# Kernel optimization log

Measured on AMD Instinct MI355X. Metric: run time of the kernel, lower is better.

The kernel has to match this reference:

```python
import jax, jax.numpy as jnp
import numpy as np

N_NODES = 100000
N_EDGES = 3200000
D_FEAT = 128
HIDDEN = 32
N_CLASS = 2


def setup_inputs() -> dict:
    key = jax.random.key(0)
    k1, k2, k3, k4 = jax.random.split(key, 4)
    x = jax.random.normal(k1, (N_NODES, D_FEAT), dtype=jnp.float32)
    edge_index = jax.random.randint(k2, (2, N_EDGES), 0, N_NODES, dtype=jnp.int64)
    W1 = jax.random.normal(k3, (D_FEAT, HIDDEN), dtype=jnp.float32) * (1.0 / np.sqrt(D_FEAT))
    b1 = jnp.zeros((HIDDEN,), dtype=jnp.float32)
    W2 = jax.random.normal(k4, (HIDDEN, N_CLASS), dtype=jnp.float32) * (1.0 / np.sqrt(HIDDEN))
    b2 = jnp.zeros((N_CLASS,), dtype=jnp.float32)
    return {"x": x, "edge_index": edge_index, "W1": W1, "b1": b1, "W2": W2, "b2": b2}


def _gcn_conv(x, src, dst, norm, W, b, n_nodes):
    # Linear transform first (PyG GCNConv order), then gather-scale-scatter.
    h = x @ W                          # [N, out]
    msg = h[src] * norm[:, None]       # [E+N, out]
    out = jax.ops.segment_sum(msg, dst, num_segments=n_nodes)
    return out + b


def reference(x, edge_index, W1, b1, W2, b2):
    n_nodes = x.shape[0]
    # Add self-loops (GCNConv default add_self_loops=True)
    loop = jnp.arange(n_nodes, dtype=edge_index.dtype)
    src = jnp.concatenate([edge_index[0], loop])
    dst = jnp.concatenate([edge_index[1], loop])
    # Symmetric normalization D^{-1/2} (A+I) D^{-1/2}; degree counted on dst.
    deg = jax.ops.segment_sum(jnp.ones_like(dst, dtype=x.dtype), dst, num_segments=n_nodes)
    deg_inv_sqrt = jnp.where(deg > 0, jax.lax.rsqrt(deg), 0.0)
    norm = deg_inv_sqrt[src] * deg_inv_sqrt[dst]   # [E+N]
    h = jax.nn.relu(_gcn_conv(x, src, dst, norm, W1, b1, n_nodes))
    # F.dropout(training=False) in eval mode is identity.
    logits = _gcn_conv(h, src, dst, norm, W2, b2, n_nodes)
    return jax.nn.log_softmax(logits, axis=1)
```

## Files before the change

kernel.cpp:

```cpp
#include <hip/hip_runtime.h>
#include <hip/hip_fp16.h>

#define NN 100000
#define NE 3200000
#define DF 128
#define HID 32
#define NC 2
#define NBUK 782
#define CAP 5376
#define PEB 8192

typedef float floatx2 __attribute__((ext_vector_type(2)));

#if defined(__has_builtin)
#if __has_builtin(__builtin_amdgcn_cvt_pk_fp8_f32) && __has_builtin(__builtin_amdgcn_cvt_pk_f32_fp8)
#define HW_FP8 1
#endif
#endif
#ifndef HW_FP8
#define HW_FP8 0
#endif

#if !HW_FP8
__device__ inline float4 e4m3x4_f4(unsigned u) {
    unsigned w0 = ((u & 0x7fu) << 7) | ((u & 0x80u) << 8)
                | ((u & 0x7f00u) << 15) | ((u & 0x8000u) << 16);
    unsigned t = u >> 16;
    unsigned w1 = ((t & 0x7fu) << 7) | ((t & 0x80u) << 8)
                | ((t & 0x7f00u) << 15) | ((t & 0x8000u) << 16);
    __half2 h0 = *reinterpret_cast<__half2*>(&w0);
    __half2 h1 = *reinterpret_cast<__half2*>(&w1);
    __half2 k = __float2half2_rn(256.f);
    float2 f0 = __half22float2(__hmul2(h0, k));
    float2 f1 = __half22float2(__hmul2(h1, k));
    return make_float4(f0.x, f0.y, f1.x, f1.y);
}
__device__ inline unsigned f2e4m3(float f) {
    unsigned u = __float_as_uint(f);
    unsigned s = (u >> 24) & 0x80u;
    int e = (int)((u >> 23) & 0xffu);
    unsigned m = u & 0x7fffffu;
    int ee = e - 120;
    if (ee >= 16) return s | 0x7eu;
    if (ee <= 0) {
        int sh = 21 - ee;
        if (sh > 31) return s;
        unsigned q = ((0x800000u | m) + (1u << (sh - 1))) >> sh;
        return s | q;
    }
    unsigned q = (m + 0x80000u) >> 20;
    if (q == 8u) { q = 0u; if (++ee >= 16) return s | 0x7eu; }
    if (ee == 15 && q == 7u) return s | 0x7eu;
    return s | ((unsigned)ee << 3) | q;
}
#endif

__device__ inline unsigned pk4_fp8(float a, float b, float c, float d) {
#if HW_FP8
    int w = 0;
    w = __builtin_amdgcn_cvt_pk_fp8_f32(a, b, w, false);
    w = __builtin_amdgcn_cvt_pk_fp8_f32(c, d, w, true);
    return (unsigned)w;
#else
    return f2e4m3(a) | (f2e4m3(b) << 8) | (f2e4m3(c) << 16) | (f2e4m3(d) << 24);
#endif
}

__global__ void k_zc(int* __restrict__ cursor) {
    int i = threadIdx.x;
    if (i < NBUK) cursor[i] = i * CAP;
}

__global__ __launch_bounds__(1024) void k_part(const int* __restrict__ eidx,
                                               int* __restrict__ cursor,
                                               unsigned* __restrict__ scr) {
    __shared__ unsigned hist[NBUK];
    __shared__ unsigned lofs[NBUK + 1];
    __shared__ unsigned aux[NBUK];
    __shared__ unsigned stage[PEB];
    __shared__ int sm[1024];
    int tid = threadIdx.x;
    int base = blockIdx.x * PEB;

    if (tid < NBUK) hist[tid] = 0u;
    __syncthreads();

    int s[PEB / 1024], d[PEB / 1024];
#pragma unroll
    for (int i = 0; i < PEB / 1024; ++i) {
        int e = base + i * 1024 + tid;
        if (e < NE) {
            s[i] = eidx[e];
            d[i] = eidx[NE + e];
            atomicAdd(&hist[d[i] >> 7], 1u);
        } else d[i] = -1;
    }
    __syncthreads();

    int v = (tid < NBUK) ? (int)hist[tid] : 0;
    sm[tid] = v;
    __syncthreads();
    for (int off = 1; off < 1024; off <<= 1) {
        int t = (tid >= off) ? sm[tid - off] : 0;
        __syncthreads();
        sm[tid] += t;
        __syncthreads();
    }
    if (tid < NBUK) {
        unsigned excl = (unsigned)(sm[tid] - v);
        lofs[tid] = excl;
        aux[tid] = excl;
    }
    if (tid == 1023) lofs[NBUK] = (unsigned)sm[1023];
    __syncthreads();

#pragma unroll
    for (int i = 0; i < PEB / 1024; ++i) {
        if (d[i] >= 0) {
            unsigned lpos = atomicAdd(&aux[d[i] >> 7], 1u);
            stage[lpos] = (unsigned)s[i] | ((unsigned)(d[i] & 127) << 17);
        }
    }
    __syncthreads();

    if (tid < NBUK) {
        unsigned c = hist[tid];
        hist[tid] = c ? (unsigned)atomicAdd(&cursor[tid], (int)c) : 0u;
    }
    __syncthreads();

    int grp = tid >> 4, lane = tid & 15;
    for (int i = grp; i < NBUK; i += 64) {
        unsigned lo = lofs[i];
        unsigned n = lofs[i + 1] - lo;
        unsigned gbase = hist[i];
        for (unsigned k = lane; k < n; k += 16)
            scr[gbase + k] = stage[lo + k];
    }
}

__global__ __launch_bounds__(256) void k_dis(const unsigned* __restrict__ scr,
                                             const int* __restrict__ cursor,
                                             float* __restrict__ dis) {
    int b = blockIdx.x;
    int cs = b * CAP, ce = cursor[b];
    __shared__ unsigned h[128];
    if (threadIdx.x < 128) h[threadIdx.x] = 0u;
    __syncthreads();
    for (int j = cs + threadIdx.x; j < ce; j += 256)
        atomicAdd(&h[(scr[j] >> 17) & 127u], 1u);
    __syncthreads();
    int r = b * 128 + threadIdx.x;
    if (threadIdx.x < 128 && r < NN)
        dis[r] = rsqrtf((float)(h[threadIdx.x] + 1u));
}

__global__ __launch_bounds__(256, 1) void k_gemm1(const float* __restrict__ x,
                                                  const float* __restrict__ dis,
                                                  const float* __restrict__ W1,
                                                  unsigned* __restrict__ h1) {
    int r = blockIdx.x * blockDim.x + threadIdx.x;
    if (r >= NN) return;
    const float4* xr = reinterpret_cast<const float4*>(x + (size_t)r * DF);
    float acc[HID];
#pragma unroll
    for (int c = 0; c < HID; ++c) acc[c] = 0.f;
#pragma unroll
    for (int kc = 0; kc < 4; ++kc) {
        float4 xq[8];
#pragma unroll
        for (int j = 0; j < 8; ++j) xq[j] = xr[kc * 8 + j];
#pragma unroll
        for (int j = 0; j < 8; ++j) {
            const float* wb = W1 + (size_t)(kc * 32 + j * 4) * HID;
#pragma unroll
            for (int c = 0; c < HID; ++c) {
                acc[c] += xq[j].x * wb[c];
                acc[c] += xq[j].y * wb[HID + c];
                acc[c] += xq[j].z * wb[2 * HID + c];
                acc[c] += xq[j].w * wb[3 * HID + c];
            }
        }
    }
    float dr = dis[r];
    unsigned w[8];
#pragma unroll
    for (int j = 0; j < 8; ++j)
        w[j] = pk4_fp8(acc[4 * j] * dr, acc[4 * j + 1] * dr,
                       acc[4 * j + 2] * dr, acc[4 * j + 3] * dr);
    uint4* dst = reinterpret_cast<uint4*>(h1 + (size_t)r * 8);
    dst[0] = make_uint4(w[0], w[1], w[2], w[3]);
    dst[1] = make_uint4(w[4], w[5], w[6], w[7]);
}

__global__ __launch_bounds__(512) void k_g1(unsigned* __restrict__ scr,
                                            const int* __restrict__ cursor,
                                            int* __restrict__ rofs, int* __restrict__ rend,
                                            const unsigned* __restrict__ h1,
                                            const float* __restrict__ b1,
                                            const float* __restrict__ W2,
                                            float* __restrict__ h2) {
    int b = blockIdx.x;
    int cs = b * CAP, ce = cursor[b];
    int n = ce - cs;
    __shared__ unsigned stage[CAP];
    __shared__ unsigned cnt[128];
    __shared__ int sm[128];
    __shared__ unsigned ofs[129];
    __shared__ float sd[128];
    int tid = threadIdx.x;

    if (tid < 128) cnt[tid] = 0u;
    __syncthreads();
    for (int j = tid; j < n; j += 512)
        atomicAdd(&cnt[(scr[cs + j] >> 17) & 127u], 1u);
    __syncthreads();
    int v = 0;
    if (tid < 128) { v = (int)cnt[tid]; sm[tid] = v; }
    __syncthreads();
    for (int off = 1; off < 128; off <<= 1) {
        int t = 0;
        if (tid < 128 && tid >= off) t = sm[tid - off];
        __syncthreads();
        if (tid < 128) sm[tid] += t;
        __syncthreads();
    }
    if (tid < 128) {
        int excl = sm[tid] - v;
        ofs[tid] = (unsigned)excl;
        cnt[tid] = (unsigned)excl;
        sd[tid] = rsqrtf((float)(v + 1));
        if (tid == 127) ofs[128] = (unsigned)(excl + v);
        int node = b * 128 + tid;
        if (node < NN) {
            rofs[node] = cs + excl;
            rend[node] = cs + excl + v;
        }
    }
    __syncthreads();
    for (int j = tid; j < n; j += 512) {
        unsigned w = scr[cs + j];
        unsigned pos = atomicAdd(&cnt[(w >> 17) & 127u], 1u);
        stage[pos] = w & 0x1FFFFu;
    }
    __syncthreads();
    for (int j = tid; j < n; j += 512) scr[cs + j] = stage[j];

    const uint2* hv = reinterpret_cast<const uint2*>(h1);
    int p = tid & 3;
    int rl = tid >> 2;
    int st = (int)ofs[rl], en = (int)ofs[rl + 1];
    float a[8];
#pragma unroll
    for (int k = 0; k < 8; ++k) a[k] = 0.f;

#if HW_FP8
#define ACC8(q)                                                               \
    {                                                                         \
        floatx2 f0 = __builtin_amdgcn_cvt_pk_f32_fp8((int)(q).x, false);      \
        floatx2 f1 = __builtin_amdgcn_cvt_pk_f32_fp8((int)(q).x, true);       \
        floatx2 f2 = __builtin_amdgcn_cvt_pk_f32_fp8((int)(q).y, false);      \
        floatx2 f3 = __builtin_amdgcn_cvt_pk_f32_fp8((int)(q).y, true);       \
        a[0] += f0.x; a[1] += f0.y; a[2] += f1.x; a[3] += f1.y;               \
        a[4] += f2.x; a[5] += f2.y; a[6] += f3.x; a[7] += f3.y;               \
    }
#else
#define ACC8(q)                                                               \
    {                                                                         \
        float4 f0 = e4m3x4_f4((q).x);                                         \
        float4 f1 = e4m3x4_f4((q).y);                                         \
        a[0] += f0.x; a[1] += f0.y; a[2] += f0.z; a[3] += f0.w;               \
        a[4] += f1.x; a[5] += f1.y; a[6] += f1.z; a[7] += f1.w;               \
    }
#endif
    int j = st;
    for (; j + 7 < en; j += 8) {
        unsigned s0 = stage[j], s1 = stage[j + 1], s2 = stage[j + 2], s3 = stage[j + 3];
        unsigned s4 = stage[j + 4], s5 = stage[j + 5], s6 = stage[j + 6], s7 = stage[j + 7];
        uint2 q0 = hv[(size_t)s0 * 4 + p];
        uint2 q1 = hv[(size_t)s1 * 4 + p];
        uint2 q2 = hv[(size_t)s2 * 4 + p];
        uint2 q3 = hv[(size_t)s3 * 4 + p];
        uint2 q4 = hv[(size_t)s4 * 4 + p];
        uint2 q5 = hv[(size_t)s5 * 4 + p];
        uint2 q6 = hv[(size_t)s6 * 4 + p];
        uint2 q7 = hv[(size_t)s7 * 4 + p];
        ACC8(q0) ACC8(q1) ACC8(q2) ACC8(q3)
        ACC8(q4) ACC8(q5) ACC8(q6) ACC8(q7)
    }
    for (; j < en; ++j) {
        uint2 q0 = hv[(size_t)stage[j] * 4 + p];
        ACC8(q0)
    }
    int rg = b * 128 + rl;
    if (rg < NN) {
        uint2 qs = hv[(size_t)rg * 4 + p];
        ACC8(qs)
        float dr = sd[rl];
        int c = p * 8;
        float4 bl = *reinterpret_cast<const float4*>(b1 + c);
        float4 bh = *reinterpret_cast<const float4*>(b1 + c + 4);
        float vv[8];
        vv[0] = fmaxf(dr * a[0] + bl.x, 0.f); vv[1] = fmaxf(dr * a[1] + bl.y, 0.f);
        vv[2] = fmaxf(dr * a[2] + bl.z, 0.f); vv[3] = fmaxf(dr * a[3] + bl.w, 0.f);
        vv[4] = fmaxf(dr * a[4] + bh.x, 0.f); vv[5] = fmaxf(dr * a[5] + bh.y, 0.f);
        vv[6] = fmaxf(dr * a[6] + bh.z, 0.f); vv[7] = fmaxf(dr * a[7] + bh.w, 0.f);
        float o0 = 0.f, o1 = 0.f;
#pragma unroll
        for (int k = 0; k < 8; ++k) {
            o0 += vv[k] * W2[(c + k) * NC + 0];
            o1 += vv[k] * W2[(c + k) * NC + 1];
        }
        o0 += __shfl_xor(o0, 1); o1 += __shfl_xor(o1, 1);
        o0 += __shfl_xor(o0, 2); o1 += __shfl_xor(o1, 2);
        if (p == 0) {
            h2[2 * (size_t)rg + 0] = dr * o0;
            h2[2 * (size_t)rg + 1] = dr * o1;
        }
    }
#undef ACC8
}

__global__ void k_gather2(const int* __restrict__ rofs, const int* __restrict__ rend,
                          const int* __restrict__ csr, const float* __restrict__ dis,
                          const float* __restrict__ h2, const float* __restrict__ b2,
                          float* __restrict__ out) {
    int r = blockIdx.x * blockDim.x + threadIdx.x;
    if (r >= NN) return;
    int start = rofs[r], end = rend[r];
    float a0 = 0.f, a1 = 0.f;
    int j = start;
    for (; j + 3 < end; j += 4) {
        int s0 = csr[j], s1 = csr[j + 1], s2 = csr[j + 2], s3 = csr[j + 3];
        float2 v0 = *(const float2*)(h2 + 2 * (size_t)s0);
        float2 v1 = *(const float2*)(h2 + 2 * (size_t)s1);
        float2 v2 = *(const float2*)(h2 + 2 * (size_t)s2);
        float2 v3 = *(const float2*)(h2 + 2 * (size_t)s3);
        a0 += v0.x + v1.x + v2.x + v3.x;
        a1 += v0.y + v1.y + v2.y + v3.y;
    }
    for (; j < end; ++j) {
        float2 v = *(const float2*)(h2 + 2 * (size_t)csr[j]);
        a0 += v.x;
        a1 += v.y;
    }
    float dr = dis[r];
    float2 own = *(const float2*)(h2 + 2 * (size_t)r);
    float l0 = dr * (a0 + own.x) + b2[0];
    float l1 = dr * (a1 + own.y) + b2[1];
    float m = fmaxf(l0, l1);
    float lse = m + logf(expf(l0 - m) + expf(l1 - m));
    out[2 * (size_t)r + 0] = l0 - lse;
    out[2 * (size_t)r + 1] = l1 - lse;
}

extern "C" void kernel_launch(void* const* d_in, const int* in_sizes, int n_in,
                              void* d_out, int out_size, void* d_ws, size_t ws_size,
                              hipStream_t stream) {
    const float* x  = (const float*)d_in[0];
    const int* ei   = (const int*)d_in[1];
    const float* W1 = (const float*)d_in[2];
    const float* b1 = (const float*)d_in[3];
    const float* W2 = (const float*)d_in[4];
    const float* b2 = (const float*)d_in[5];
    float* out      = (float*)d_out;

    float* ws     = (float*)d_ws;
    float* dis    = ws;
    int* rofs     = (int*)(ws + (size_t)NN);
    int* rend     = (int*)(ws + (size_t)2 * NN);
    int* cursor   = (int*)(ws + (size_t)3 * NN);
    float* h2     = ws + (size_t)3 * NN + 800;
    unsigned* h1  = (unsigned*)(ws + (size_t)5 * NN + 800);
    unsigned* scr = (unsigned*)(ws + (size_t)13 * NN + 800);

    k_zc<<<1, 1024, 0, stream>>>(cursor);
    k_part<<<(NE + PEB - 1) / PEB, 1024, 0, stream>>>(ei, cursor, scr);
    k_dis<<<NBUK, 256, 0, stream>>>(scr, cursor, dis);
    k_gemm1<<<(NN + 255) / 256, 256, 0, stream>>>(x, dis, W1, h1);
    k_g1<<<NBUK, 512, 0, stream>>>(scr, cursor, rofs, rend, h1, b1, W2, h2);
    k_gather2<<<(NN + 255) / 256, 256, 0, stream>>>(rofs, rend, (const int*)scr, dis, h2, b2, out);
}
```

Measured before the change: 114.3 us.

## Split gemm1 K dimension across four waves with LDS reduction

The first linear layer previously had each thread compute one full 128-wide row, giving only 391 blocks capped at one block per CU. It now assigns 64 rows per block and splits the K dimension across four wavefronts. Partial sums are reduced through shared memory, and four threads per row pack and store the fp8 output. This gives four times as many blocks and more latency hiding for the x loads, at the cost of an LDS round trip and a barrier.

After: 147.1 us. +28.8%, slower.

```diff
diff --git a/kernel.cpp b/kernel.cpp
--- a/kernel.cpp
+++ b/kernel.cpp
@@ -155,42 +155,51 @@
         dis[r] = rsqrtf((float)(h[threadIdx.x] + 1u));
 }
 
-__global__ __launch_bounds__(256, 1) void k_gemm1(const float* __restrict__ x,
-                                                  const float* __restrict__ dis,
-                                                  const float* __restrict__ W1,
-                                                  unsigned* __restrict__ h1) {
-    int r = blockIdx.x * blockDim.x + threadIdx.x;
-    if (r >= NN) return;
-    const float4* xr = reinterpret_cast<const float4*>(x + (size_t)r * DF);
+__global__ __launch_bounds__(256) void k_gemm1(const float* __restrict__ x,
+                                               const float* __restrict__ dis,
+                                               const float* __restrict__ W1,
+                                               unsigned* __restrict__ h1) {
+    __shared__ float red[4][64][33];
+    int tid = threadIdx.x;
+    int w = tid >> 6, l = tid & 63;
+    int r0 = blockIdx.x * 64;
+    int rl = r0 + l;
+    int rc = (rl < NN) ? rl : (NN - 1);
+    const float4* xr = reinterpret_cast<const float4*>(x + (size_t)rc * DF) + w * 8;
+    float4 xq[8];
+#pragma unroll
+    for (int j = 0; j < 8; ++j) xq[j] = xr[j];
     float acc[HID];
 #pragma unroll
     for (int c = 0; c < HID; ++c) acc[c] = 0.f;
 #pragma unroll
-    for (int kc = 0; kc < 4; ++kc) {
-        float4 xq[8];
-#pragma unroll
-        for (int j = 0; j < 8; ++j) xq[j] = xr[kc * 8 + j];
+    for (int j = 0; j < 8; ++j) {
+        const float* wr = W1 + (size_t)(w * 32 + j * 4) * HID;
+#pragma unroll
+        for (int c = 0; c < HID; ++c) {
+            acc[c] += xq[j].x * wr[c];
+            acc[c] += xq[j].y * wr[HID + c];
+            acc[c] += xq[j].z * wr[2 * HID + c];
+            acc[c] += xq[j].w * wr[3 * HID + c];
+        }
+    }
+#pragma unroll
+    for (int c = 0; c < HID; ++c) red[w][l][c] = acc[c];
+    __syncthreads();
+    int row = tid >> 2, p = tid & 3;
+    int rg = r0 + row;
+    if (rg < NN) {
+        float dr = dis[rg];
+        float s[8];
 #pragma unroll
         for (int j = 0; j < 8; ++j) {
-            const float* wb = W1 + (size_t)(kc * 32 + j * 4) * HID;
-#pragma unroll
-            for (int c = 0; c < HID; ++c) {
-                acc[c] += xq[j].x * wb[c];
-                acc[c] += xq[j].y * wb[HID + c];
-                acc[c] += xq[j].z * wb[2 * HID + c];
-                acc[c] += xq[j].w * wb[3 * HID + c];
-            }
-        }
-    }
-    float dr = dis[r];
-    unsigned w[8];
-#pragma unroll
-    for (int j = 0; j < 8; ++j)
-        w[j] = pk4_fp8(acc[4 * j] * dr, acc[4 * j + 1] * dr,
-                       acc[4 * j + 2] * dr, acc[4 * j + 3] * dr);
-    uint4* dst = reinterpret_cast<uint4*>(h1 + (size_t)r * 8);
-    dst[0] = make_uint4(w[0], w[1], w[2], w[3]);
-    dst[1] = make_uint4(w[4], w[5], w[6], w[7]);
+            int c = p * 8 + j;
+            s[j] = (red[0][row][c] + red[1][row][c]) + (red[2][row][c] + red[3][row][c]);
+        }
+        unsigned lo = pk4_fp8(s[0] * dr, s[1] * dr, s[2] * dr, s[3] * dr);
+        unsigned hi = pk4_fp8(s[4] * dr, s[5] * dr, s[6] * dr, s[7] * dr);
+        reinterpret_cast<uint2*>(h1)[(size_t)rg * 4 + p] = make_uint2(lo, hi);
+    }
 }
 
 __global__ __launch_bounds__(512) void k_g1(unsigned* __restrict__ scr,
@@ -377,7 +386,7 @@
     k_zc<<<1, 1024, 0, stream>>>(cursor);
     k_part<<<(NE + PEB - 1) / PEB, 1024, 0, stream>>>(ei, cursor, scr);
     k_dis<<<NBUK, 256, 0, stream>>>(scr, cursor, dis);
-    k_gemm1<<<(NN + 255) / 256, 256, 0, stream>>>(x, dis, W1, h1);
+    k_gemm1<<<(NN + 63) / 64, 256, 0, stream>>>(x, dis, W1, h1);
     k_g1<<<NBUK, 512, 0, stream>>>(scr, cursor, rofs, rend, h1, b1, W2, h2);
     k_gather2<<<(NN + 255) / 256, 256, 0, stream>>>(rofs, rend, (const int*)scr, dis, h2, b2, out);
 }
```
